# Kernel optimization log

Measured on AMD Instinct MI355X. Metric: run time of the kernel, lower is better.

The kernel has to match this reference:

```python
import jax, jax.numpy as jnp
import numpy as np

L, NB, B, S, D = 4, 8, 16, 512, 512   # layers, blocks/pathway, batch, seq, dim
K = 2            # max_active_blocks (top-k routing)
FUSION = 0.3     # fusion_strength
PRIOR = 0.5      # fresh block priority: 0.5*0.6 + 0.5*0.4
EPS = 1e-5


def setup_inputs() -> dict:
    key = jax.random.key(0)
    ks = jax.random.split(key, 16)
    rn = lambda k, shp, s=0.02: jax.random.normal(k, shp, dtype=jnp.float32) * s
    return {
        'cortical_input': rn(ks[0], (B, S, D), 1.0),
        'brainstem_input': rn(ks[1], (B, S, D), 1.0),
        'torsion_field': rn(ks[2], (1, D), 1.0),
        'w_sel_c': rn(ks[3], (L, D, NB)), 'b_sel_c': jnp.zeros((L, NB), jnp.float32),
        'w_sel_b': rn(ks[4], (L, D, NB)), 'b_sel_b': jnp.zeros((L, NB), jnp.float32),
        'c_ln_g': jnp.ones((L, NB, D), jnp.float32), 'c_ln_b': jnp.zeros((L, NB, D), jnp.float32),
        'c_w1': rn(ks[5], (L, NB, D, 2 * D)), 'c_b1': jnp.zeros((L, NB, 2 * D), jnp.float32),
        'c_w2': rn(ks[6], (L, NB, 2 * D, D)), 'c_b2': jnp.zeros((L, NB, D), jnp.float32),
        'c_gate': rn(ks[7], (L, NB, D), 0.01),
        'b_ln_g': jnp.ones((L, NB, D), jnp.float32), 'b_ln_b': jnp.zeros((L, NB, D), jnp.float32),
        'b_w1': rn(ks[8], (L, NB, D, D)), 'b_b1': jnp.zeros((L, NB, D), jnp.float32),
        'b_w2': rn(ks[9], (L, NB, D, D)), 'b_b2': jnp.zeros((L, NB, D), jnp.float32),
        'b_gate': rn(ks[10], (L, NB, D), 0.01),
        'w_cross': rn(ks[11], (L, 2 * D, D)), 'b_cross': jnp.zeros((L, D), jnp.float32),
    }


def _block(x, torsion, signal, g, beta, w1, b1, w2, b2, gate, act):
    # LayerNorm -> MLP -> torsion gate -> cross-pathway fusion -> residual*0.5
    mu = x.mean(-1, keepdims=True)
    var = ((x - mu) ** 2).mean(-1, keepdims=True)
    h = (x - mu) * jax.lax.rsqrt(var + EPS) * g + beta
    h = act(h @ w1 + b1) @ w2 + b2
    tg = jax.nn.sigmoid(gate)                 # [D]
    h = h * (1.0 + (tg * torsion)[:, None, :])  # torsion_field: [1,D] -> [1,1,D]
    h = h + signal * tg                        # pathway_signal [B,1,D] * fusion_weight [D]
    return x + 0.5 * h


def _pathway(x, other, torsion, wsel, bsel, g, beta, w1, b1, w2, b2, gate, act):
    scores = jax.nn.sigmoid(x.mean(1) @ wsel + bsel)     # [B, NB]
    adjusted = scores[0] * 0.7 + PRIOR * 0.3             # routing uses sample 0
    _, top = jax.lax.top_k(adjusted, K)
    signal = other.mean(1, keepdims=True) * FUSION       # [B,1,D]
    h = x
    for j in range(K):  # sequential application of the K selected blocks
        i = top[j]
        h = _block(h, torsion, signal, g[i], beta[i], w1[i], b1[i], w2[i], b2[i], gate[i], act)
    return h


def _forward(cortical_input, brainstem_input, torsion_field,
             w_sel_c, b_sel_c, w_sel_b, b_sel_b,
             c_ln_g, c_ln_b, c_w1, c_b1, c_w2, c_b2, c_gate,
             b_ln_g, b_ln_b, b_w1, b_b1, b_w2, b_b2, b_gate,
             w_cross, b_cross):
    c, b = cortical_input, brainstem_input
    gelu = lambda v: jax.nn.gelu(v, approximate=False)
    fused = None
    for l in range(L):
        c_in, b_in = c, b
        c = _pathway(c_in, b_in, torsion_field, w_sel_c[l], b_sel_c[l],
                     c_ln_g[l], c_ln_b[l], c_w1[l], c_b1[l], c_w2[l], c_b2[l], c_gate[l], gelu)
        b = _pathway(b_in, c_in, torsion_field, w_sel_b[l], b_sel_b[l],
                     b_ln_g[l], b_ln_b[l], b_w1[l], b_b1[l], b_w2[l], b_b2[l], b_gate[l], jnp.tanh)
        fused = jnp.concatenate([c, b], axis=-1) @ w_cross[l] + b_cross[l]
    return c, b, fused


def reference(cortical_input, brainstem_input, torsion_field,
              w_sel_c, b_sel_c, w_sel_b, b_sel_b,
              c_ln_g, c_ln_b, c_w1, c_b1, c_w2, c_b2, c_gate,
              b_ln_g, b_ln_b, b_w1, b_b1, b_w2, b_b2, b_gate,
              w_cross, b_cross):
    return _forward(cortical_input, brainstem_input, torsion_field,
                    w_sel_c, b_sel_c, w_sel_b, b_sel_b,
                    c_ln_g, c_ln_b, c_w1, c_b1, c_w2, c_b2, c_gate,
                    b_ln_g, b_ln_b, b_w1, b_b1, b_w2, b_b2, b_gate,
                    w_cross, b_cross)
```

## Files before the change

kernel.cpp:

```cpp
#include <hip/hip_runtime.h>
#include <hip/hip_bf16.h>
#include <math.h>

typedef short s16x8 __attribute__((ext_vector_type(8)));
typedef float f32x4 __attribute__((ext_vector_type(4)));
typedef unsigned short u16;

#define NB_ 8

__device__ __forceinline__ float bf2f(__hip_bfloat16 v){ return __bfloat162float(v); }
__device__ __forceinline__ __hip_bfloat16 f2bf(float v){ return __float2bfloat16(v); }
__device__ __forceinline__ u16 f2u(float v){ __hip_bfloat16 b = f2bf(v); return *(u16*)&b; }

__device__ __forceinline__ float fsigm(float x){ return 1.0f / (1.0f + __expf(-x)); }
__device__ __forceinline__ float ftanh(float x){ return 1.0f - 2.0f / (__expf(2.0f * x) + 1.0f); }
__device__ __forceinline__ float fgelu(float x){
    return 0.5f * x * (1.0f + ftanh(0.79788456080286536f * (x + 0.044715f * x * x * x)));
}

__device__ __forceinline__ void async16(u16* lds, const u16* g)
{
    __builtin_amdgcn_global_load_lds((const __attribute__((address_space(1))) void*)g,
                                     (__attribute__((address_space(3))) void*)lds,
                                     16, 0, 0);
}

struct GArg {
    const u16* A0; const u16* A1; int lda; int ksplit;
    const u16* BT; const float* bias; int bias_stride;
    const float* gate; int gate_stride; const float* meansig;
    u16* outb; float* xio; int N; int K; int idx_off; int mode;
};

__global__ __launch_bounds__(256)
void gemm_dual(GArg ga, GArg gb, int ysplit,
               const int* __restrict__ idxbuf, const float* __restrict__ torsion)
{
    __shared__ __align__(16) u16 As[2][128 * 64];
    __shared__ __align__(16) u16 Bs[2][128 * 64];
    const bool second = (int)blockIdx.y >= ysplit;
    const GArg& g = second ? gb : ga;
    const int n0 = (second ? blockIdx.y - ysplit : blockIdx.y) * 128;
    const int m0 = blockIdx.x * 128;
    const int tid = threadIdx.x;
    const int wave = tid >> 6, lane = tid & 63;
    const int wm = (wave >> 1) * 64, wn = (wave & 1) * 64;
    const int lrow = lane & 15, quad = lane >> 4;

    int rS[4], cS[4];
#pragma unroll
    for (int it = 0; it < 4; it++) {
        int s = wave * 2048 + it * 512 + lane * 8;
        rS[it] = s >> 6;
        cS[it] = ((((s >> 3) & 7) ^ (rS[it] & 7)) << 3);
    }

    f32x4 acc[4][4] = {};
    const int K = g.K, ksplit = g.ksplit, lda = g.lda, N = g.N;
    const u16* BTn = g.BT + (size_t)n0 * K;
    const int niter = K >> 6;

    auto stage = [&](int k0, int buf) {
        const u16* Ab; int kk;
        if (k0 < ksplit) { Ab = g.A0; kk = k0; }
        else             { Ab = g.A1; kk = k0 - ksplit; }
        const u16* Arow = Ab + (size_t)m0 * lda + kk;
        u16* Ad = &As[buf][wave * 2048];
        u16* Bd = &Bs[buf][wave * 2048];
#pragma unroll
        for (int it = 0; it < 4; it++)
            async16(Ad + it * 512, Arow + (size_t)rS[it] * lda + cS[it]);
#pragma unroll
        for (int it = 0; it < 4; it++)
            async16(Bd + it * 512, BTn + (size_t)rS[it] * K + k0 + cS[it]);
    };

    stage(0, 0);
    __syncthreads();

    for (int k = 0; k < niter; k++) {
        int cur = k & 1, nxt = cur ^ 1;
        if (k + 1 < niter) stage((k + 1) << 6, nxt);
#pragma unroll
        for (int ks = 0; ks < 64; ks += 32) {
            s16x8 af[4], bfv[4];
#pragma unroll
            for (int i = 0; i < 4; i++) {
                int r = wm + i * 16 + lrow;
                int cp = (((ks >> 3) + quad) ^ (r & 7)) << 3;
                af[i] = *(const s16x8*)&As[cur][r * 64 + cp];
            }
#pragma unroll
            for (int j = 0; j < 4; j++) {
                int r = wn + j * 16 + lrow;
                int cp = (((ks >> 3) + quad) ^ (r & 7)) << 3;
                bfv[j] = *(const s16x8*)&Bs[cur][r * 64 + cp];
            }
#pragma unroll
            for (int i = 0; i < 4; i++)
#pragma unroll
                for (int j = 0; j < 4; j++)
                    acc[i][j] = __builtin_amdgcn_mfma_f32_16x16x32_bf16(af[i], bfv[j], acc[i][j], 0, 0, 0);
        }
        __syncthreads();
    }

    const int idx = (g.idx_off >= 0) ? idxbuf[g.idx_off] : 0;
    const float* bias = g.bias + (size_t)idx * g.bias_stride;
    const float* gate = g.gate ? (g.gate + (size_t)idx * g.gate_stride) : nullptr;
    const float* msrow = g.meansig ? (g.meansig + (size_t)(m0 >> 9) * 512) : nullptr;
    const int mode = g.mode;

#pragma unroll
    for (int j = 0; j < 4; j++) {
        const int n = n0 + wn + j * 16 + lrow;
        const float bn = bias[n];
        float ea = 0.f, ec = 0.f;
        if (mode == 2) {
            float tg  = fsigm(gate[n]);
            float tor = torsion[n];
            ea = 0.5f * (1.0f + tg * tor);
            ec = 0.5f * (msrow[n] * 0.3f) * tg;
        }
#pragma unroll
        for (int i = 0; i < 4; i++) {
#pragma unroll
            for (int r = 0; r < 4; r++) {
                const int m = m0 + wm + i * 16 + quad * 4 + r;
                const size_t off = (size_t)m * N + n;
                float v = acc[i][j][r] + bn;
                if (mode == 0)      g.outb[off] = f2u(fgelu(v));
                else if (mode == 1) g.outb[off] = f2u(ftanh(v));
                else if (mode == 2) g.xio[off] = g.xio[off] + ea * v + ec;
                else                g.xio[off] = v;
            }
        }
    }
}

__global__ __launch_bounds__(64)
void ln_dual(const float* __restrict__ xc, const float* __restrict__ xb,
             u16* __restrict__ lnc, u16* __restrict__ lnb,
             const float* __restrict__ cg, const float* __restrict__ cb,
             const float* __restrict__ bg, const float* __restrict__ bb,
             const int* __restrict__ idxbuf, int j)
{
    int bid = blockIdx.x, lane = threadIdx.x;
    bool second = bid >= 8192;
    int row = second ? bid - 8192 : bid;
    const float* x = second ? xb : xc;
    u16* out = second ? lnb : lnc;
    const float* gbase = second ? bg : cg;
    const float* bbase = second ? bb : cb;
    int idx = idxbuf[second ? 2 + j : j];

    const float* xr = x + (size_t)row * 512;
    float4 v0 = *(const float4*)(xr + lane * 8);
    float4 v1 = *(const float4*)(xr + lane * 8 + 4);
    float vals[8] = {v0.x, v0.y, v0.z, v0.w, v1.x, v1.y, v1.z, v1.w};
    float s = 0.f, s2 = 0.f;
#pragma unroll
    for (int t = 0; t < 8; t++) { s += vals[t]; s2 += vals[t] * vals[t]; }
#pragma unroll
    for (int o = 32; o; o >>= 1) { s += __shfl_xor(s, o); s2 += __shfl_xor(s2, o); }
    float mu  = s * (1.f / 512.f);
    float var = s2 * (1.f / 512.f) - mu * mu;
    float rs  = rsqrtf(var + 1e-5f);
    const float* gg  = gbase + (size_t)idx * 512;
    const float* bbp = bbase + (size_t)idx * 512;
    int d0 = lane * 8;
    __align__(16) u16 o8[8];
#pragma unroll
    for (int t = 0; t < 8; t++)
        o8[t] = f2u((vals[t] - mu) * rs * gg[d0 + t] + bbp[d0 + t]);
    *(uint4*)(out + (size_t)row * 512 + d0) = *(const uint4*)o8;
}

__global__ void zero_kernel(float* p, int n)
{
    int i = blockIdx.x * blockDim.x + threadIdx.x;
    if (i < n) p[i] = 0.f;
}

__global__ __launch_bounds__(512)
void mean_kernel(const float* __restrict__ xc, const float* __restrict__ xb,
                 float* __restrict__ mc, float* __restrict__ mb)
{
    int bid = blockIdx.x;
    int half = bid >> 7;
    const float* x = half ? xb : xc;
    float* m = half ? mb : mc;
    int b = (bid & 127) >> 3, ch = bid & 7;
    int d = threadIdx.x;
    const float* p = x + ((size_t)b * 512 + ch * 64) * 512 + d;
    float s = 0.f;
#pragma unroll 8
    for (int i = 0; i < 64; i++) s += p[(size_t)i * 512];
    atomicAdd(&m[b * 512 + d], s * (1.f / 512.f));
}

__global__ __launch_bounds__(128)
void route_kernel(const float* __restrict__ mc, const float* __restrict__ mb,
                  const float* __restrict__ wsel_c, const float* __restrict__ bsel_c,
                  const float* __restrict__ wsel_b, const float* __restrict__ bsel_b,
                  int* __restrict__ idx_out)
{
    int g = threadIdx.x >> 6, lane = threadIdx.x & 63;
    const float* mrow = g ? mb : mc;
    const float* ws = g ? wsel_b : wsel_c;
    const float* bs = g ? bsel_b : bsel_c;
    float acc[8] = {0.f, 0.f, 0.f, 0.f, 0.f, 0.f, 0.f, 0.f};
    for (int d = lane; d < 512; d += 64) {
        float mv = mrow[d];
#pragma unroll
        for (int n = 0; n < 8; n++) acc[n] += mv * ws[d * 8 + n];
    }
#pragma unroll
    for (int o = 32; o; o >>= 1)
#pragma unroll
        for (int n = 0; n < 8; n++) acc[n] += __shfl_xor(acc[n], o);
    if (lane == 0) {
        float adj[8];
#pragma unroll
        for (int n = 0; n < 8; n++) {
            float sc = 1.0f / (1.0f + expf(-(acc[n] + bs[n])));
            adj[n] = 0.7f * sc + 0.15f;
        }
        int i0 = 0;
        for (int n = 1; n < 8; n++) if (adj[n] > adj[i0]) i0 = n;
        int i1 = -1;
        for (int n = 0; n < 8; n++) {
            if (n == i0) continue;
            if (i1 < 0 || adj[n] > adj[i1]) i1 = n;
        }
        idx_out[g * 2 + 0] = i0;
        idx_out[g * 2 + 1] = i1;
    }
}

struct TArg { const float* src; u16* dst; int R; int C; int idx_off; int nblk; };

__global__ __launch_bounds__(256)
void transpose4(TArg t0, TArg t1, TArg t2, TArg t3, const int* __restrict__ idxbuf)
{
    int bid = blockIdx.x;
    TArg t;
    if (bid < t0.nblk) t = t0;
    else { bid -= t0.nblk;
        if (bid < t1.nblk) t = t1;
        else { bid -= t1.nblk;
            if (bid < t2.nblk) t = t2;
            else { bid -= t2.nblk; t = t3; } } }
    int idx = (t.idx_off >= 0) ? idxbuf[t.idx_off] : 0;
    const float* src = t.src + (size_t)idx * t.R * t.C;
    int tpr = t.C >> 5;
    int tr = bid / tpr, tc = bid % tpr;
    __shared__ u16 tile[32][33];
    int tx = threadIdx.x & 31, ty = threadIdx.x >> 5;
#pragma unroll
    for (int r = ty; r < 32; r += 8)
        tile[r][tx] = f2u(src[(size_t)(tr * 32 + r) * t.C + tc * 32 + tx]);
    __syncthreads();
#pragma unroll
    for (int r = ty; r < 32; r += 8)
        t.dst[(size_t)(tc * 32 + r) * t.R + tr * 32 + tx] = tile[tx][r];
}

__global__ __launch_bounds__(256)
void f2b_kernel(const float* __restrict__ xa, const float* __restrict__ xb,
                u16* __restrict__ oa, u16* __restrict__ ob)
{
    int i = (blockIdx.x * 256 + threadIdx.x) * 8;
    const float* src = blockIdx.y ? xb : xa;
    u16* dst = blockIdx.y ? ob : oa;
    float4 f0 = *(const float4*)(src + i);
    float4 f1 = *(const float4*)(src + i + 4);
    float vv[8] = {f0.x, f0.y, f0.z, f0.w, f1.x, f1.y, f1.z, f1.w};
    __align__(16) u16 o8[8];
#pragma unroll
    for (int t = 0; t < 8; t++) o8[t] = f2u(vv[t]);
    *(uint4*)(dst + i) = *(const uint4*)o8;
}

extern "C" void kernel_launch(void* const* d_in, const int* in_sizes, int n_in,
                              void* d_out, int out_size, void* d_ws, size_t ws_size,
                              hipStream_t stream)
{
    const float* in_c   = (const float*)d_in[0];
    const float* in_b   = (const float*)d_in[1];
    const float* torsion= (const float*)d_in[2];
    const float* wsel_c = (const float*)d_in[3];
    const float* bsel_c = (const float*)d_in[4];
    const float* wsel_b = (const float*)d_in[5];
    const float* bsel_b = (const float*)d_in[6];
    const float* c_ln_g = (const float*)d_in[7];
    const float* c_ln_b = (const float*)d_in[8];
    const float* c_w1   = (const float*)d_in[9];
    const float* c_b1   = (const float*)d_in[10];
    const float* c_w2   = (const float*)d_in[11];
    const float* c_b2   = (const float*)d_in[12];
    const float* c_gate = (const float*)d_in[13];
    const float* b_ln_g = (const float*)d_in[14];
    const float* b_ln_b = (const float*)d_in[15];
    const float* b_w1   = (const float*)d_in[16];
    const float* b_b1   = (const float*)d_in[17];
    const float* b_w2   = (const float*)d_in[18];
    const float* b_b2   = (const float*)d_in[19];
    const float* b_gate = (const float*)d_in[20];
    const float* w_cross= (const float*)d_in[21];
    const float* b_cross= (const float*)d_in[22];

    const size_t SD = (size_t)8192 * 512;

    float* x_c  = (float*)d_out;
    float* x_b  = x_c + SD;
    float* out_f = x_b + SD;

    char* w = (char*)d_ws;
    u16* lnc   = (u16*)w; w += SD * 2;
    u16* lnb   = (u16*)w; w += SD * 2;
    u16* act_c = (u16*)w; w += SD * 2 * 2;
    u16* act_b = (u16*)w; w += SD * 2;
    u16* cbf   = (u16*)w; w += SD * 2;
    u16* bbf   = (u16*)w; w += SD * 2;
    float* mean_c = (float*)w; w += (size_t)16 * 512 * 4;
    float* mean_b = (float*)w; w += (size_t)16 * 512 * 4;
    int*   idxbuf = (int*)w;   w += 256;
    u16* w1t_c = (u16*)w; w += (size_t)1024 * 512 * 2;
    u16* w2t_c = (u16*)w; w += (size_t)1024 * 512 * 2;
    u16* w1t_b = (u16*)w; w += (size_t)512 * 512 * 2;
    u16* w2t_b = (u16*)w; w += (size_t)512 * 512 * 2;
    u16* wxT   = (u16*)w; w += (size_t)1024 * 512 * 2;

    hipMemcpyAsync(x_c, in_c, SD * 4, hipMemcpyDeviceToDevice, stream);
    hipMemcpyAsync(x_b, in_b, SD * 4, hipMemcpyDeviceToDevice, stream);

    TArg twx = { w_cross + (size_t)3 * 1024 * 512, wxT, 1024, 512, -1, 512 };
    TArg tz  = { nullptr, nullptr, 32, 32, -1, 0 };
    transpose4<<<512, 256, 0, stream>>>(twx, tz, tz, tz, idxbuf);

    for (int l = 0; l < 4; l++) {
        zero_kernel<<<64, 256, 0, stream>>>(mean_c, 16384);
        mean_kernel<<<256, 512, 0, stream>>>(x_c, x_b, mean_c, mean_b);
        route_kernel<<<1, 128, 0, stream>>>(mean_c, mean_b,
            wsel_c + (size_t)l * 512 * 8, bsel_c + (size_t)l * 8,
            wsel_b + (size_t)l * 512 * 8, bsel_b + (size_t)l * 8, idxbuf);

        for (int j = 0; j < 2; j++) {
            TArg tc1 = { c_w1 + (size_t)l * NB_ * 512 * 1024, w1t_c, 512, 1024, j, 512 };
            TArg tc2 = { c_w2 + (size_t)l * NB_ * 1024 * 512, w2t_c, 1024, 512, j, 512 };
            TArg tb1 = { b_w1 + (size_t)l * NB_ * 512 * 512,  w1t_b, 512, 512, 2 + j, 256 };
            TArg tb2 = { b_w2 + (size_t)l * NB_ * 512 * 512,  w2t_b, 512, 512, 2 + j, 256 };
            transpose4<<<1536, 256, 0, stream>>>(tc1, tc2, tb1, tb2, idxbuf);

            ln_dual<<<16384, 64, 0, stream>>>(x_c, x_b, lnc, lnb,
                c_ln_g + (size_t)l * NB_ * 512, c_ln_b + (size_t)l * NB_ * 512,
                b_ln_g + (size_t)l * NB_ * 512, b_ln_b + (size_t)l * NB_ * 512,
                idxbuf, j);

            GArg g1c = { lnc, nullptr, 512, 1 << 30, w1t_c,
                         c_b1 + (size_t)l * NB_ * 1024, 1024,
                         nullptr, 0, nullptr, act_c, nullptr, 1024, 512, j, 0 };
            GArg g1b = { lnb, nullptr, 512, 1 << 30, w1t_b,
                         b_b1 + (size_t)l * NB_ * 512, 512,
                         nullptr, 0, nullptr, act_b, nullptr, 512, 512, 2 + j, 1 };
            gemm_dual<<<dim3(64, 12), 256, 0, stream>>>(g1c, g1b, 8, idxbuf, torsion);

            GArg g2c = { act_c, nullptr, 1024, 1 << 30, w2t_c,
                         c_b2 + (size_t)l * NB_ * 512, 512,
                         c_gate + (size_t)l * NB_ * 512, 512, mean_b,
                         nullptr, x_c, 512, 1024, j, 2 };
            GArg g2b = { act_b, nullptr, 512, 1 << 30, w2t_b,
                         b_b2 + (size_t)l * NB_ * 512, 512,
                         b_gate + (size_t)l * NB_ * 512, 512, mean_c,
                         nullptr, x_b, 512, 512, 2 + j, 2 };
            gemm_dual<<<dim3(64, 8), 256, 0, stream>>>(g2c, g2b, 4, idxbuf, torsion);
        }
    }

    f2b_kernel<<<dim3(2048, 2), 256, 0, stream>>>(x_c, x_b, cbf, bbf);
    GArg gf = { cbf, bbf, 512, 512, wxT,
                b_cross + (size_t)3 * 512, 0,
                nullptr, 0, nullptr, nullptr, out_f, 512, 1024, -1, 3 };
    gemm_dual<<<dim3(64, 4), 256, 0, stream>>>(gf, gf, 4, idxbuf, torsion);
}
```

Before: 1.087 ms.

## Halve GEMM K-tile, drop LDS swizzle, stage bf16 epilogue through LDS

The GEMM K-step shrinks from 64 to 32, which cuts shared memory per block from 64KB to 32KB. Launch bounds now request 4 blocks per CU, trading more barriers per K and less prefetch depth for higher occupancy. The XOR swizzle on the A/B tiles is removed, which may introduce LDS bank conflicts on the fragment reads. For the gelu/tanh modes the epilogue writes bf16 results into a swizzled LDS tile and then stores coalesced 16-byte rows to global memory, replacing scattered 2-byte stores.

```diff
diff --git a/kernel.cpp b/kernel.cpp
--- a/kernel.cpp
+++ b/kernel.cpp
@@ -32,12 +32,11 @@
     u16* outb; float* xio; int N; int K; int idx_off; int mode;
 };
 
-__global__ __launch_bounds__(256)
+__global__ __launch_bounds__(256, 4)
 void gemm_dual(GArg ga, GArg gb, int ysplit,
                const int* __restrict__ idxbuf, const float* __restrict__ torsion)
 {
-    __shared__ __align__(16) u16 As[2][128 * 64];
-    __shared__ __align__(16) u16 Bs[2][128 * 64];
+    __shared__ __align__(16) u16 sm[4][128 * 32];
     const bool second = (int)blockIdx.y >= ysplit;
     const GArg& g = second ? gb : ga;
     const int n0 = (second ? blockIdx.y - ysplit : blockIdx.y) * 128;
@@ -47,31 +46,31 @@
     const int wm = (wave >> 1) * 64, wn = (wave & 1) * 64;
     const int lrow = lane & 15, quad = lane >> 4;
 
-    int rS[4], cS[4];
-#pragma unroll
-    for (int it = 0; it < 4; it++) {
-        int s = wave * 2048 + it * 512 + lane * 8;
-        rS[it] = s >> 6;
-        cS[it] = ((((s >> 3) & 7) ^ (rS[it] & 7)) << 3);
+    int rS[2], cS[2];
+#pragma unroll
+    for (int it = 0; it < 2; it++) {
+        int s = wave * 1024 + it * 512 + lane * 8;
+        rS[it] = s >> 5;
+        cS[it] = s & 31;
     }
 
     f32x4 acc[4][4] = {};
     const int K = g.K, ksplit = g.ksplit, lda = g.lda, N = g.N;
     const u16* BTn = g.BT + (size_t)n0 * K;
-    const int niter = K >> 6;
+    const int niter = K >> 5;
 
     auto stage = [&](int k0, int buf) {
         const u16* Ab; int kk;
         if (k0 < ksplit) { Ab = g.A0; kk = k0; }
         else             { Ab = g.A1; kk = k0 - ksplit; }
         const u16* Arow = Ab + (size_t)m0 * lda + kk;
-        u16* Ad = &As[buf][wave * 2048];
-        u16* Bd = &Bs[buf][wave * 2048];
-#pragma unroll
-        for (int it = 0; it < 4; it++)
+        u16* Ad = &sm[buf][wave * 1024];
+        u16* Bd = &sm[2 + buf][wave * 1024];
+#pragma unroll
+        for (int it = 0; it < 2; it++)
             async16(Ad + it * 512, Arow + (size_t)rS[it] * lda + cS[it]);
 #pragma unroll
-        for (int it = 0; it < 4; it++)
+        for (int it = 0; it < 2; it++)
             async16(Bd + it * 512, BTn + (size_t)rS[it] * K + k0 + cS[it]);
     };
 
@@ -80,28 +79,19 @@
 
     for (int k = 0; k < niter; k++) {
         int cur = k & 1, nxt = cur ^ 1;
-        if (k + 1 < niter) stage((k + 1) << 6, nxt);
-#pragma unroll
-        for (int ks = 0; ks < 64; ks += 32) {
-            s16x8 af[4], bfv[4];
-#pragma unroll
-            for (int i = 0; i < 4; i++) {
-                int r = wm + i * 16 + lrow;
-                int cp = (((ks >> 3) + quad) ^ (r & 7)) << 3;
-                af[i] = *(const s16x8*)&As[cur][r * 64 + cp];
-            }
-#pragma unroll
-            for (int j = 0; j < 4; j++) {
-                int r = wn + j * 16 + lrow;
-                int cp = (((ks >> 3) + quad) ^ (r & 7)) << 3;
-                bfv[j] = *(const s16x8*)&Bs[cur][r * 64 + cp];
-            }
-#pragma unroll
-            for (int i = 0; i < 4; i++)
-#pragma unroll
-                for (int j = 0; j < 4; j++)
-                    acc[i][j] = __builtin_amdgcn_mfma_f32_16x16x32_bf16(af[i], bfv[j], acc[i][j], 0, 0, 0);
-        }
+        if (k + 1 < niter) stage((k + 1) << 5, nxt);
+        s16x8 af[4], bfv[4];
+#pragma unroll
+        for (int i = 0; i < 4; i++)
+            af[i] = *(const s16x8*)&sm[cur][(wm + i * 16 + lrow) * 32 + quad * 8];
+#pragma unroll
+        for (int j = 0; j < 4; j++)
+            bfv[j] = *(const s16x8*)&sm[2 + cur][(wn + j * 16 + lrow) * 32 + quad * 8];
+#pragma unroll
+        for (int i = 0; i < 4; i++)
+#pragma unroll
+            for (int j = 0; j < 4; j++)
+                acc[i][j] = __builtin_amdgcn_mfma_f32_16x16x32_bf16(af[i], bfv[j], acc[i][j], 0, 0, 0);
         __syncthreads();
     }
 
@@ -110,6 +100,35 @@
     const float* gate = g.gate ? (g.gate + (size_t)idx * g.gate_stride) : nullptr;
     const float* msrow = g.meansig ? (g.meansig + (size_t)(m0 >> 9) * 512) : nullptr;
     const int mode = g.mode;
+
+    if (mode <= 1) {
+        u16* CT = &sm[0][0];
+#pragma unroll
+        for (int j = 0; j < 4; j++) {
+            const int n_loc = wn + j * 16 + lrow;
+            const float bn = bias[n0 + n_loc];
+#pragma unroll
+            for (int i = 0; i < 4; i++) {
+#pragma unroll
+                for (int r = 0; r < 4; r++) {
+                    const int m_loc = wm + i * 16 + quad * 4 + r;
+                    float v = acc[i][j][r] + bn;
+                    v = (mode == 0) ? fgelu(v) : ftanh(v);
+                    CT[m_loc * 128 + (n_loc ^ (quad << 4))] = f2u(v);
+                }
+            }
+        }
+        __syncthreads();
+#pragma unroll
+        for (int p = 0; p < 8; p++) {
+            int ip  = p * 256 + tid;
+            int row = ip >> 4;
+            int c0  = (ip & 15) * 8;
+            s16x8 vv = *(const s16x8*)&CT[row * 128 + (c0 ^ (((row >> 2) & 3) << 4))];
+            *(s16x8*)&g.outb[(size_t)(m0 + row) * N + n0 + c0] = vv;
+        }
+        return;
+    }
 
 #pragma unroll
     for (int j = 0; j < 4; j++) {
@@ -129,10 +148,8 @@
                 const int m = m0 + wm + i * 16 + quad * 4 + r;
                 const size_t off = (size_t)m * N + n;
                 float v = acc[i][j][r] + bn;
-                if (mode == 0)      g.outb[off] = f2u(fgelu(v));
-                else if (mode == 1) g.outb[off] = f2u(ftanh(v));
-                else if (mode == 2) g.xio[off] = g.xio[off] + ea * v + ec;
-                else                g.xio[off] = v;
+                if (mode == 2) g.xio[off] = g.xio[off] + ea * v + ec;
+                else           g.xio[off] = v;
             }
         }
     }
```

New measurement: 954.3 us. 1.14x faster.
